# Performance work log

Measured on AMD Instinct MI355X. Metric: run time of the kernel, lower is better.

The kernel has to match this reference:

```python
import jax, jax.numpy as jnp
import numpy as np

N_NODES = 100000
N_EDGES = 1600000
N_GRAPHS = 64
FEAT = 64
EMB = 64
HID = 64
VOCAB = 32


def setup_inputs() -> dict:
    key = jax.random.key(0)
    ks = jax.random.split(key, 20)
    w = lambda k, sh: (jax.random.normal(k, sh, jnp.float32) * 0.05)
    x = jax.random.normal(ks[0], (N_NODES, FEAT), jnp.float32)
    edge_index = jax.random.randint(ks[1], (2, N_EDGES), 0, N_NODES, dtype=jnp.int32).astype(jnp.int64)
    batch = jnp.sort(jax.random.randint(ks[2], (N_NODES,), 0, N_GRAPHS, dtype=jnp.int32)).astype(jnp.int64)
    return {
        'x': x, 'edge_index': edge_index, 'batch': batch,
        # RGCN layer 1 (single relation): relation weight, root weight, bias
        'W1': w(ks[3], (FEAT, EMB)), 'root1': w(ks[4], (FEAT, EMB)), 'b1': w(ks[5], (EMB,)),
        # RGCN layer 2
        'W2': w(ks[6], (EMB, HID)), 'root2': w(ks[7], (EMB, HID)), 'b2': w(ks[8], (HID,)),
        # init_h / init_c linear heads
        'Wh': w(ks[9], (HID, HID)), 'bh': w(ks[10], (HID,)),
        'Wc': w(ks[11], (HID, HID)), 'bc': w(ks[12], (HID,)),
        # output layer
        'Wo': w(ks[13], (HID, VOCAB)), 'bo': w(ks[14], (VOCAB,)),
    }


def _rgcn(x, edge_index, W, root, b):
    # PyG RGCNConv with num_relations=1, aggr='mean':
    # out[i] = mean_{j in N(i)} (x[j] @ W) + x[i] @ root + b
    src, dst = edge_index[0], edge_index[1]
    msg = x[src] @ W                                    # [E, out] gather + small GEMM
    agg = jax.ops.segment_sum(msg, dst, num_segments=x.shape[0])
    cnt = jax.ops.segment_sum(jnp.ones((edge_index.shape[1],), x.dtype), dst, num_segments=x.shape[0])
    agg = agg / jnp.maximum(cnt, 1.0)[:, None]
    return agg + x @ root + b


def reference(x, edge_index, batch, W1, root1, b1, W2, root2, b2, Wh, bh, Wc, bc, Wo, bo):
    h = jax.nn.relu(_rgcn(x, edge_index, W1, root1, b1))
    h = jax.nn.relu(_rgcn(h, edge_index, W2, root2, b2))
    # global_mean_pool over graph-assignment vector `batch`
    summ = jax.ops.segment_sum(h, batch, num_segments=N_GRAPHS)
    cnt = jax.ops.segment_sum(jnp.ones((h.shape[0],), h.dtype), batch, num_segments=N_GRAPHS)
    pooled = summ / jnp.maximum(cnt, 1.0)[:, None]      # [G, HID]
    hidden = pooled @ Wh + bh
    cell = pooled @ Wc + bc
    logits = jax.nn.log_softmax(hidden @ Wo + bo, axis=1)
    return (logits, hidden, cell)
```

## Files before the change

kernel.cpp:

```cpp
#include <hip/hip_runtime.h>
#include <hip/hip_bf16.h>


typedef __attribute__((ext_vector_type(8))) short short8;
typedef __attribute__((ext_vector_type(4))) float f32x4;
typedef __attribute__((ext_vector_type(2))) float f32x2;

#define RB 9
#define MAXBINS 256
#define CAP 12288
#define BCAP 14336
#define CHUNK 8192

__device__ inline float bf2f(unsigned short h) {
    return __uint_as_float(((unsigned int)h) << 16);
}
__device__ inline float bflo(unsigned int u) { return __uint_as_float(u << 16); }
__device__ inline float bfhi(unsigned int u) { return __uint_as_float(u & 0xffff0000u); }
__device__ inline unsigned short f2bf(float f) {
    unsigned int u = __float_as_uint(f);
    u = (u + 0x7fffu + ((u >> 16) & 1u)) >> 16;
    return (unsigned short)u;
}

__device__ inline void build_bfrag(const float* __restrict__ W,
                                   const float* __restrict__ R,
                                   int q, int mm, short8 bfrag[8][2]) {
#pragma unroll
    for (int t = 0; t < 8; ++t) {
        const int n = t * 16 + mm;
        const float* P = (n < 64) ? (W + n) : (R + n - 64);
#pragma unroll
        for (int c = 0; c < 2; ++c) {
#pragma unroll
            for (int j = 0; j < 8; ++j) {
                const int k = c * 32 + q * 8 + j;
                bfrag[t][c][j] = (short)f2bf(P[k * 64]);
            }
        }
    }
}

__device__ inline void store_xw_fp8(unsigned char* __restrict__ xw8, int rowbase, int q,
                                    int t, int mm, const f32x4& accT, int N) {
#pragma unroll
    for (int r = 0; r < 4; ++r) {
        const float v0 = accT[r];
        const float v1 = __shfl_down(v0, 1);
        const float v2 = __shfl_down(v0, 2);
        const float v3 = __shfl_down(v0, 3);
        const int orow = rowbase + q * 4 + r;
        if (!(mm & 3) && orow < N) {
            unsigned int u = (unsigned int)__builtin_amdgcn_cvt_pk_fp8_f32(v0, v1, 0, false);
            u = (unsigned int)__builtin_amdgcn_cvt_pk_fp8_f32(v2, v3, (int)u, true);
            *(unsigned int*)&xw8[(size_t)orow * 64 + t * 16 + mm] = u;
        }
    }
}

__global__ __launch_bounds__(256) void bin_gemm1(const int* __restrict__ src,
                                                 const int* __restrict__ dst,
                                                 unsigned int* __restrict__ coarse,
                                                 int* __restrict__ gcur,
                                                 int E, int BINS, int nbBin,
                                                 const float* __restrict__ x,
                                                 const float* __restrict__ W1,
                                                 const float* __restrict__ R1,
                                                 const float* __restrict__ bias,
                                                 unsigned char* __restrict__ xw8,
                                                 unsigned short* __restrict__ xrb,
                                                 int N) {
    __shared__ int cnt[MAXBINS];
    __shared__ int incl[MAXBINS];
    __shared__ int bstart[MAXBINS];
    __shared__ int bcur[MAXBINS];
    __shared__ int gbase[MAXBINS];
    __shared__ unsigned int stage[CHUNK];
    __shared__ unsigned char binOf[CHUNK];

    const int tid = threadIdx.x;
    if (blockIdx.x >= (unsigned)nbBin) {
        const int gb = blockIdx.x - nbBin;
        if (gb == 0 && tid < 16)
            *(unsigned int*)&xw8[(size_t)N * 64 + tid * 4] = 0u;

        const int lane = tid & 63;
        const int q = lane >> 4;
        const int mm = lane & 15;

        short8 bfrag[8][2];
        build_bfrag(W1, R1, q, mm, bfrag);
        float bv[4];
#pragma unroll
        for (int tt = 0; tt < 4; ++tt) bv[tt] = bias[tt * 16 + mm];

        const int wid = tid >> 6;
        const int gw = gb * 4 + wid;
        const int nw = 1024 * 4;
        const int ntiles = N >> 4;

        for (int tile = gw; tile < ntiles; tile += nw) {
            const int row0 = tile << 4;
            const float* ap = &x[(size_t)(row0 + mm) * 64 + q * 8];
            const float4 f0 = *(const float4*)ap;
            const float4 f1 = *(const float4*)(ap + 4);
            const float4 f2 = *(const float4*)(ap + 32);
            const float4 f3 = *(const float4*)(ap + 36);
            short8 a0, a1;
            a0[0] = (short)f2bf(f0.x); a0[1] = (short)f2bf(f0.y);
            a0[2] = (short)f2bf(f0.z); a0[3] = (short)f2bf(f0.w);
            a0[4] = (short)f2bf(f1.x); a0[5] = (short)f2bf(f1.y);
            a0[6] = (short)f2bf(f1.z); a0[7] = (short)f2bf(f1.w);
            a1[0] = (short)f2bf(f2.x); a1[1] = (short)f2bf(f2.y);
            a1[2] = (short)f2bf(f2.z); a1[3] = (short)f2bf(f2.w);
            a1[4] = (short)f2bf(f3.x); a1[5] = (short)f2bf(f3.y);
            a1[6] = (short)f2bf(f3.z); a1[7] = (short)f2bf(f3.w);
            f32x4 acc[8];
#pragma unroll
            for (int t = 0; t < 8; ++t) {
                acc[t] = (f32x4){0.f, 0.f, 0.f, 0.f};
                acc[t] = __builtin_amdgcn_mfma_f32_16x16x32_bf16(a0, bfrag[t][0], acc[t], 0, 0, 0);
                acc[t] = __builtin_amdgcn_mfma_f32_16x16x32_bf16(a1, bfrag[t][1], acc[t], 0, 0, 0);
            }
#pragma unroll
            for (int t = 0; t < 4; ++t) store_xw_fp8(xw8, row0, q, t, mm, acc[t], N);
#pragma unroll
            for (int t = 4; t < 8; ++t) {
#pragma unroll
                for (int r = 0; r < 4; ++r) {
                    const float v = acc[t][r] + bv[t - 4];
                    const float vn = __shfl_down(v, 1);
                    if (!(mm & 1)) {
                        const unsigned int u = (unsigned int)f2bf(v) | ((unsigned int)f2bf(vn) << 16);
                        *(unsigned int*)&xrb[(size_t)(row0 + q * 4 + r) * 64 + (t - 4) * 16 + mm] = u;
                    }
                }
            }
        }
        return;
    }

    const int chunk0 = blockIdx.x * CHUNK;
    int myS[32], myD[32];
#pragma unroll
    for (int k = 0; k < 32; ++k) {
        const int idx = chunk0 + k * 256 + tid;
        if (idx < E) { myS[k] = src[idx]; myD[k] = dst[idx]; }
        else myD[k] = -1;
    }
    cnt[tid] = 0;
    __syncthreads();
#pragma unroll
    for (int k = 0; k < 32; ++k)
        if (myD[k] >= 0) atomicAdd(&cnt[myD[k] >> RB], 1);
    __syncthreads();
    incl[tid] = cnt[tid];
    __syncthreads();
    for (int off = 1; off < 256; off <<= 1) {
        int t = (tid >= off) ? incl[tid - off] : 0;
        __syncthreads();
        incl[tid] += t;
        __syncthreads();
    }
    bstart[tid] = incl[tid] - cnt[tid];
    bcur[tid] = incl[tid] - cnt[tid];
    __syncthreads();
#pragma unroll
    for (int k = 0; k < 32; ++k) {
        if (myD[k] >= 0) {
            const int b = myD[k] >> RB;
            const int pos = atomicAdd(&bcur[b], 1);
            stage[pos] = (unsigned int)myS[k] | ((unsigned int)(myD[k] & ((1 << RB) - 1)) << 17);
            binOf[pos] = (unsigned char)b;
        }
    }
    __syncthreads();
    if (tid < BINS && cnt[tid] > 0)
        gbase[tid] = tid * CAP + atomicAdd(&gcur[tid], cnt[tid]);
    __syncthreads();
    int total = E - chunk0;
    if (total > CHUNK) total = CHUNK;
    for (int idx = tid; idx < total; idx += 256) {
        const int b = binOf[idx];
        coarse[gbase[b] + (idx - bstart[b])] = stage[idx];
    }
}

__global__ __launch_bounds__(256) void finalize_csr(const unsigned int* __restrict__ coarse,
                                                    const int* __restrict__ gcur,
                                                    int* __restrict__ bucket,
                                                    int* __restrict__ pstart,
                                                    int* __restrict__ degarr,
                                                    int N, int BINS) {
    __shared__ int ncnt[512];
    __shared__ int pexcl[512];
    __shared__ int ncur[512];
    __shared__ int s2[256];

    const int tid = threadIdx.x;
    const int b = blockIdx.x;
    const int cb = gcur[b];
    const int base = b * BCAP;
    const unsigned int* reg = coarse + (size_t)b * CAP;
    const int node0 = b << RB;
    int nloc = N - node0;
    if (nloc > 512) nloc = 512;

    ncnt[tid] = 0; ncnt[tid + 256] = 0;
    __syncthreads();
    for (int idx = tid; idx < cb; idx += 256)
        atomicAdd(&ncnt[reg[idx] >> 17], 1);
    __syncthreads();
    const int p0 = (ncnt[2 * tid] + 15) & ~15;
    const int p1 = (ncnt[2 * tid + 1] + 15) & ~15;
    s2[tid] = p0 + p1;
    __syncthreads();
    for (int off = 1; off < 256; off <<= 1) {
        int t = (tid >= off) ? s2[tid - off] : 0;
        __syncthreads();
        s2[tid] += t;
        __syncthreads();
    }
    const int pairExcl = s2[tid] - (p0 + p1);
    pexcl[2 * tid] = pairExcl;
    pexcl[2 * tid + 1] = pairExcl + p0;
    ncur[2 * tid] = pairExcl;
    ncur[2 * tid + 1] = pairExcl + p0;
    __syncthreads();
    for (int i = tid; i < nloc; i += 256) {
        pstart[node0 + i] = base + pexcl[i];
        degarr[node0 + i] = ncnt[i];
        const int dg = ncnt[i];
        const int pd = (dg + 15) & ~15;
        for (int j = dg; j < pd; ++j) bucket[base + pexcl[i] + j] = N;
    }
    for (int idx = tid; idx < cb; idx += 256) {
        const unsigned int e = reg[idx];
        const int p = atomicAdd(&ncur[e >> 17], 1);
        bucket[base + p] = (int)(e & 0x1FFFFu);
    }
}

__global__ __launch_bounds__(256) void aggregate(const unsigned char* __restrict__ xw8,
                                                 const unsigned short* __restrict__ xrb,
                                                 const int* __restrict__ pstart,
                                                 const int* __restrict__ degarr,
                                                 const int* __restrict__ bucket,
                                                 unsigned short* __restrict__ outb,
                                                 int N) {
    const int lane = threadIdx.x & 63;
    const int quarter = lane >> 4;
    const int fl = lane & 15;
    const int wid = threadIdx.x >> 6;
    const int gw = blockIdx.x * 4 + wid;
    const int nw = gridDim.x * 4;

    for (int i = gw; i < N; i += nw) {
        const int r0 = pstart[i];
        const int dg = degarr[i];
        const int pdeg = (dg + 15) & ~15;
        float a0 = 0.f, a1 = 0.f, a2 = 0.f, a3 = 0.f;
        for (int base = 0; base < pdeg; base += 64) {
            const int rem = pdeg - base;
            const int s = (lane < rem) ? bucket[r0 + base + lane] : N;
            const int mm = rem < 64 ? rem : 64;
            for (int t = 0; t < mm; t += 16) {
                unsigned int u[4];
#pragma unroll
                for (int p = 0; p < 4; ++p) {
                    const int rr = __shfl(s, t + 4 * p + quarter);
                    u[p] = *(const unsigned int*)&xw8[(size_t)rr * 64 + fl * 4];
                }
#pragma unroll
                for (int p = 0; p < 4; ++p) {
                    const f32x2 lo = __builtin_amdgcn_cvt_pk_f32_fp8(u[p], false);
                    const f32x2 hi = __builtin_amdgcn_cvt_pk_f32_fp8(u[p], true);
                    a0 += lo.x; a1 += lo.y; a2 += hi.x; a3 += hi.y;
                }
            }
        }
        a0 += __shfl_xor(a0, 16); a1 += __shfl_xor(a1, 16);
        a2 += __shfl_xor(a2, 16); a3 += __shfl_xor(a3, 16);
        a0 += __shfl_xor(a0, 32); a1 += __shfl_xor(a1, 32);
        a2 += __shfl_xor(a2, 32); a3 += __shfl_xor(a3, 32);

        const float inv = 1.0f / (float)(dg > 0 ? dg : 1);
        if (quarter == 0) {
            const uint2 ur = *(const uint2*)&xrb[(size_t)i * 64 + fl * 4];
            const float o0 = fmaxf(a0 * inv + bflo(ur.x), 0.f);
            const float o1 = fmaxf(a1 * inv + bfhi(ur.x), 0.f);
            const float o2 = fmaxf(a2 * inv + bflo(ur.y), 0.f);
            const float o3 = fmaxf(a3 * inv + bfhi(ur.y), 0.f);
            uint2 w;
            w.x = (unsigned int)f2bf(o0) | ((unsigned int)f2bf(o1) << 16);
            w.y = (unsigned int)f2bf(o2) | ((unsigned int)f2bf(o3) << 16);
            *(uint2*)&outb[(size_t)i * 64 + fl * 4] = w;
        }
    }
}

__global__ __launch_bounds__(256) void gemm_xwr2(const unsigned short* __restrict__ xin,
                                                 const float* __restrict__ W2,
                                                 const float* __restrict__ R2,
                                                 const float* __restrict__ bias,
                                                 unsigned char* __restrict__ xw8,
                                                 unsigned short* __restrict__ xrb,
                                                 int M) {
    if (blockIdx.x == 0 && threadIdx.x < 16)
        *(unsigned int*)&xw8[(size_t)M * 64 + threadIdx.x * 4] = 0u;

    const int lane = threadIdx.x & 63;
    const int q = lane >> 4;
    const int mm = lane & 15;

    short8 bfrag[8][2];
    build_bfrag(W2, R2, q, mm, bfrag);
    float bv[4];
#pragma unroll
    for (int tt = 0; tt < 4; ++tt) bv[tt] = bias[tt * 16 + mm];

    const int wid = threadIdx.x >> 6;
    const int gw = blockIdx.x * 4 + wid;
    const int nw = gridDim.x * 4;
    const int ntiles = M >> 4;

    for (int tile = gw; tile < ntiles; tile += nw) {
        const int row0 = tile << 4;
        const short8 a0 = *(const short8*)&xin[(size_t)(row0 + mm) * 64 + q * 8];
        const short8 a1 = *(const short8*)&xin[(size_t)(row0 + mm) * 64 + 32 + q * 8];
        f32x4 acc[8];
#pragma unroll
        for (int t = 0; t < 8; ++t) {
            acc[t] = (f32x4){0.f, 0.f, 0.f, 0.f};
            acc[t] = __builtin_amdgcn_mfma_f32_16x16x32_bf16(a0, bfrag[t][0], acc[t], 0, 0, 0);
            acc[t] = __builtin_amdgcn_mfma_f32_16x16x32_bf16(a1, bfrag[t][1], acc[t], 0, 0, 0);
        }
#pragma unroll
        for (int t = 0; t < 4; ++t) store_xw_fp8(xw8, row0, q, t, mm, acc[t], M);
#pragma unroll
        for (int t = 4; t < 8; ++t) {
#pragma unroll
            for (int r = 0; r < 4; ++r) {
                const float v = acc[t][r] + bv[t - 4];
                const float vn = __shfl_down(v, 1);
                if (!(mm & 1)) {
                    const unsigned int u = (unsigned int)f2bf(v) | ((unsigned int)f2bf(vn) << 16);
                    *(unsigned int*)&xrb[(size_t)(row0 + q * 4 + r) * 64 + (t - 4) * 16 + mm] = u;
                }
            }
        }
    }
}

__global__ __launch_bounds__(256) void pool_kernel(const unsigned short* __restrict__ h,
                                                   const int* __restrict__ batch,
                                                   float* __restrict__ pooled, int N) {
    __shared__ float red[16][64];
    __shared__ int bnds[2];
    const int gph = blockIdx.x;
    if (threadIdx.x < 2) {
        const int target = gph + threadIdx.x;
        int lo = 0, hi = N;
        while (lo < hi) {
            int mid = (lo + hi) >> 1;
            if (batch[mid] < target) lo = mid + 1; else hi = mid;
        }
        bnds[threadIdx.x] = lo;
    }
    __syncthreads();
    const int r0 = bnds[0], r1 = bnds[1];
    const int f = threadIdx.x & 15;
    const int r = threadIdx.x >> 4;
    float4 acc = {0.f, 0.f, 0.f, 0.f};
    for (int row = r0 + r; row < r1; row += 16) {
        const ushort4 v = *(const ushort4*)&h[(size_t)row * 64 + f * 4];
        acc.x += bf2f(v.x); acc.y += bf2f(v.y);
        acc.z += bf2f(v.z); acc.w += bf2f(v.w);
    }
    red[r][f * 4 + 0] = acc.x; red[r][f * 4 + 1] = acc.y;
    red[r][f * 4 + 2] = acc.z; red[r][f * 4 + 3] = acc.w;
    __syncthreads();
    if (threadIdx.x < 64) {
        float s = 0.f;
        for (int j = 0; j < 16; ++j) s += red[j][threadIdx.x];
        const int cnt = r1 - r0;
        const float invc = 1.0f / (float)(cnt > 0 ? cnt : 1);
        pooled[gph * 64 + threadIdx.x] = s * invc;
    }
}

__global__ __launch_bounds__(256) void head_kernel(const float* __restrict__ pooled,
                                                   const float* __restrict__ Wh,
                                                   const float* __restrict__ bh,
                                                   const float* __restrict__ Wc,
                                                   const float* __restrict__ bc,
                                                   const float* __restrict__ Wo,
                                                   const float* __restrict__ bo,
                                                   float* __restrict__ out) {
    __shared__ float pm[4096];
    __shared__ float Ws[4096];
    __shared__ float Cs[4096];
    __shared__ float hid[4096];
    const int t = threadIdx.x;

    for (int idx = t; idx < 1024; idx += 256) {
        ((float4*)pm)[idx] = ((const float4*)pooled)[idx];
        ((float4*)Ws)[idx] = ((const float4*)Wh)[idx];
        ((float4*)Cs)[idx] = ((const float4*)Wc)[idx];
    }
    __syncthreads();

    const int w = t >> 6;
    const int l = t & 63;
    const float bhv = bh[l], bcv = bc[l];
    float ah[16], ac[16];
#pragma unroll
    for (int i = 0; i < 16; ++i) { ah[i] = bhv; ac[i] = bcv; }
    const float* pmw = pm + ((w << 4) << 6);
#pragma unroll 4
    for (int k = 0; k < 64; ++k) {
        const float wv = Ws[(k << 6) + l];
        const float cv = Cs[(k << 6) + l];
#pragma unroll
        for (int i = 0; i < 16; ++i) {
            const float p = pmw[(i << 6) + k];
            ah[i] = fmaf(p, wv, ah[i]);
            ac[i] = fmaf(p, cv, ac[i]);
        }
    }
#pragma unroll
    for (int i = 0; i < 16; ++i) {
        const int g = (w << 4) + i;
        hid[(g << 6) + l] = ah[i];
        out[2048 + (g << 6) + l] = ah[i];
        out[6144 + (g << 6) + l] = ac[i];
    }
    __syncthreads();
    for (int idx = t; idx < 512; idx += 256)
        ((float4*)Ws)[idx] = ((const float4*)Wo)[idx];
    __syncthreads();

    const int v = l & 31;
    const int gh = l >> 5;
    const int g0 = ((w << 1) + gh) << 3;
    const float bov = bo[v];
    float lgacc[8];
#pragma unroll
    for (int i = 0; i < 8; ++i) lgacc[i] = bov;
#pragma unroll 4
    for (int k = 0; k < 64; ++k) {
        const float wv = Ws[(k << 5) + v];
#pragma unroll
        for (int i = 0; i < 8; ++i)
            lgacc[i] = fmaf(hid[((g0 + i) << 6) + k], wv, lgacc[i]);
    }
    float* lg = pm;
#pragma unroll
    for (int i = 0; i < 8; ++i) lg[((g0 + i) << 5) + v] = lgacc[i];
    __syncthreads();

    const int g = t >> 2;
    const int vs = (t & 3) << 3;
    const float* row = lg + (g << 5);
    float mx = -3.4e38f;
#pragma unroll
    for (int j = 0; j < 8; ++j) mx = fmaxf(mx, row[vs + j]);
    mx = fmaxf(mx, __shfl_xor(mx, 1));
    mx = fmaxf(mx, __shfl_xor(mx, 2));
    float s = 0.f;
#pragma unroll
    for (int j = 0; j < 8; ++j) s += __expf(row[vs + j] - mx);
    s += __shfl_xor(s, 1);
    s += __shfl_xor(s, 2);
    const float lse = mx + __logf(s);
#pragma unroll
    for (int j = 0; j < 8; ++j) out[(g << 5) + vs + j] = row[vs + j] - lse;
}

extern "C" void kernel_launch(void* const* d_in, const int* in_sizes, int n_in,
                              void* d_out, int out_size, void* d_ws, size_t ws_size,
                              hipStream_t stream) {
    const float* x = (const float*)d_in[0];
    const int* ei = (const int*)d_in[1];
    const int* batch = (const int*)d_in[2];
    const float* W1 = (const float*)d_in[3];
    const float* root1 = (const float*)d_in[4];
    const float* b1 = (const float*)d_in[5];
    const float* W2 = (const float*)d_in[6];
    const float* root2 = (const float*)d_in[7];
    const float* b2 = (const float*)d_in[8];
    const float* Wh = (const float*)d_in[9];
    const float* bh = (const float*)d_in[10];
    const float* Wc = (const float*)d_in[11];
    const float* bc = (const float*)d_in[12];
    const float* Wo = (const float*)d_in[13];
    const float* bo = (const float*)d_in[14];
    float* out = (float*)d_out;

    const int N = in_sizes[0] / 64;
    const int E = in_sizes[1] / 2;
    const int* srcp = ei;
    const int* dstp = ei + E;
    const int BINS = (N + (1 << RB) - 1) >> RB;

    char* ws = (char*)d_ws;
    size_t off = 0;
    auto alloc = [&](size_t bytes) -> void* {
        void* p = ws + off;
        off += (bytes + 255) & ~(size_t)255;
        return p;
    };
    int* pstart = (int*)alloc((size_t)N * 4);
    int* degarr = (int*)alloc((size_t)N * 4);
    int* bucket = (int*)alloc(((size_t)BINS * BCAP + 256) * 4);
    unsigned int* coarse = (unsigned int*)alloc((size_t)BINS * CAP * 4);
    unsigned short* h1 = (unsigned short*)alloc((size_t)N * 64 * 2);
    unsigned short* h2 = (unsigned short*)alloc((size_t)N * 64 * 2);
    unsigned char* xw8 = (unsigned char*)alloc((size_t)(N + 1) * 64);
    unsigned char* xw8b = (unsigned char*)alloc((size_t)(N + 1) * 64);
    unsigned short* xrb = (unsigned short*)alloc((size_t)N * 64 * 2);
    unsigned short* xrb2 = (unsigned short*)alloc((size_t)N * 64 * 2);
    float* pooled = (float*)alloc(4096 * 4);
    int* gcur = (int*)alloc(MAXBINS * 4);

    const int nbBin = (E + CHUNK - 1) / CHUNK;

    hipMemsetAsync(gcur, 0, MAXBINS * 4, stream);
    bin_gemm1<<<nbBin + 1024, 256, 0, stream>>>(srcp, dstp, coarse, gcur, E, BINS, nbBin,
                                                x, W1, root1, b1, xw8, xrb, N);
    finalize_csr<<<BINS, 256, 0, stream>>>(coarse, gcur, bucket, pstart, degarr, N, BINS);
    aggregate<<<4096, 256, 0, stream>>>(xw8, xrb, pstart, degarr, bucket, h1, N);
    gemm_xwr2<<<1024, 256, 0, stream>>>(h1, W2, root2, b2, xw8b, xrb2, N);
    aggregate<<<4096, 256, 0, stream>>>(xw8b, xrb2, pstart, degarr, bucket, h2, N);
    pool_kernel<<<64, 256, 0, stream>>>(h2, batch, pooled, N);
    head_kernel<<<1, 256, 0, stream>>>(pooled, Wh, bh, Wc, bc, Wo, bo, out);
}
```

Baseline: 272.0 us.

## Fuse layer-1 aggregation with layer-2 GEMM and layer-2 aggregation with pooling

Layer-1 neighbour aggregation now writes each 16-row tile into LDS and immediately feeds it to the MFMA transform for layer 2, removing the h1 buffer round trip. Layer-2 aggregation accumulates per-graph sums over contiguous node ranges and flushes them with atomics, removing h2 and the separate pooling kernel; the head kernel now computes graph counts and normalizes. This cuts global traffic and launches but serializes 16 rows per wave in the first fused kernel, which may reduce latency hiding, and introduces float atomics.

Result: slower. 348.5 us (+28.1%).

```diff
diff --git a/kernel.cpp b/kernel.cpp
--- a/kernel.cpp
+++ b/kernel.cpp
@@ -241,21 +241,149 @@
     }
 }
 
-__global__ __launch_bounds__(256) void aggregate(const unsigned char* __restrict__ xw8,
+__global__ __launch_bounds__(256) void agg1_gemm2(const unsigned char* __restrict__ xw8,
+                                                  const unsigned short* __restrict__ xrb,
+                                                  const int* __restrict__ pstart,
+                                                  const int* __restrict__ degarr,
+                                                  const int* __restrict__ bucket,
+                                                  const float* __restrict__ W2,
+                                                  const float* __restrict__ R2,
+                                                  const float* __restrict__ bias,
+                                                  unsigned char* __restrict__ xw8b,
+                                                  unsigned short* __restrict__ xrb2,
+                                                  int N) {
+    if (blockIdx.x == 0 && threadIdx.x < 16)
+        *(unsigned int*)&xw8b[(size_t)N * 64 + threadIdx.x * 4] = 0u;
+
+    __shared__ unsigned short tile[4][16 * 72];
+
+    const int lane = threadIdx.x & 63;
+    const int quarter = lane >> 4;
+    const int fl = lane & 15;
+    const int wid = threadIdx.x >> 6;
+
+    short8 bfrag[8][2];
+    build_bfrag(W2, R2, quarter, fl, bfrag);
+    float bv[4];
+#pragma unroll
+    for (int tt = 0; tt < 4; ++tt) bv[tt] = bias[tt * 16 + fl];
+
+    const int gw = blockIdx.x * 4 + wid;
+    const int nw = gridDim.x * 4;
+    const int ntiles = (N + 15) >> 4;
+    unsigned short* my = tile[wid];
+
+    for (int tl = gw; tl < ntiles; tl += nw) {
+        const int row0 = tl << 4;
+        for (int r = 0; r < 16; ++r) {
+            const int i = row0 + r;
+            float a0 = 0.f, a1 = 0.f, a2 = 0.f, a3 = 0.f;
+            int dg = 0;
+            if (i < N) {
+                const int r0 = pstart[i];
+                dg = degarr[i];
+                const int pdeg = (dg + 15) & ~15;
+                for (int base = 0; base < pdeg; base += 64) {
+                    const int rem = pdeg - base;
+                    const int s = (lane < rem) ? bucket[r0 + base + lane] : N;
+                    const int mx = rem < 64 ? rem : 64;
+                    for (int tq = 0; tq < mx; tq += 16) {
+                        unsigned int u[4];
+#pragma unroll
+                        for (int p = 0; p < 4; ++p) {
+                            const int rr = __shfl(s, tq + 4 * p + quarter);
+                            u[p] = *(const unsigned int*)&xw8[(size_t)rr * 64 + fl * 4];
+                        }
+#pragma unroll
+                        for (int p = 0; p < 4; ++p) {
+                            const f32x2 lo = __builtin_amdgcn_cvt_pk_f32_fp8(u[p], false);
+                            const f32x2 hi = __builtin_amdgcn_cvt_pk_f32_fp8(u[p], true);
+                            a0 += lo.x; a1 += lo.y; a2 += hi.x; a3 += hi.y;
+                        }
+                    }
+                }
+                a0 += __shfl_xor(a0, 16); a1 += __shfl_xor(a1, 16);
+                a2 += __shfl_xor(a2, 16); a3 += __shfl_xor(a3, 16);
+                a0 += __shfl_xor(a0, 32); a1 += __shfl_xor(a1, 32);
+                a2 += __shfl_xor(a2, 32); a3 += __shfl_xor(a3, 32);
+            }
+            if (quarter == 0) {
+                uint2 w = {0u, 0u};
+                if (i < N) {
+                    const float inv = 1.0f / (float)(dg > 0 ? dg : 1);
+                    const uint2 ur = *(const uint2*)&xrb[(size_t)i * 64 + fl * 4];
+                    const float o0 = fmaxf(a0 * inv + bflo(ur.x), 0.f);
+                    const float o1 = fmaxf(a1 * inv + bfhi(ur.x), 0.f);
+                    const float o2 = fmaxf(a2 * inv + bflo(ur.y), 0.f);
+                    const float o3 = fmaxf(a3 * inv + bfhi(ur.y), 0.f);
+                    w.x = (unsigned int)f2bf(o0) | ((unsigned int)f2bf(o1) << 16);
+                    w.y = (unsigned int)f2bf(o2) | ((unsigned int)f2bf(o3) << 16);
+                }
+                *(uint2*)&my[r * 72 + fl * 4] = w;
+            }
+        }
+        asm volatile("s_waitcnt lgkmcnt(0)" ::: "memory");
+        __builtin_amdgcn_sched_barrier(0);
+        const short8 a0v = *(const short8*)&my[fl * 72 + quarter * 8];
+        const short8 a1v = *(const short8*)&my[fl * 72 + 32 + quarter * 8];
+        f32x4 acc[8];
+#pragma unroll
+        for (int t = 0; t < 8; ++t) {
+            acc[t] = (f32x4){0.f, 0.f, 0.f, 0.f};
+            acc[t] = __builtin_amdgcn_mfma_f32_16x16x32_bf16(a0v, bfrag[t][0], acc[t], 0, 0, 0);
+            acc[t] = __builtin_amdgcn_mfma_f32_16x16x32_bf16(a1v, bfrag[t][1], acc[t], 0, 0, 0);
+        }
+#pragma unroll
+        for (int t = 0; t < 4; ++t) store_xw_fp8(xw8b, row0, quarter, t, fl, acc[t], N);
+#pragma unroll
+        for (int t = 4; t < 8; ++t) {
+#pragma unroll
+            for (int r2 = 0; r2 < 4; ++r2) {
+                const float v = acc[t][r2] + bv[t - 4];
+                const float vn = __shfl_down(v, 1);
+                const int orow = row0 + quarter * 4 + r2;
+                if (!(fl & 1) && orow < N) {
+                    const unsigned int u = (unsigned int)f2bf(v) | ((unsigned int)f2bf(vn) << 16);
+                    *(unsigned int*)&xrb2[(size_t)orow * 64 + (t - 4) * 16 + fl] = u;
+                }
+            }
+        }
+    }
+}
+
+__global__ __launch_bounds__(256) void agg2_pool(const unsigned char* __restrict__ xw8,
                                                  const unsigned short* __restrict__ xrb,
                                                  const int* __restrict__ pstart,
                                                  const int* __restrict__ degarr,
                                                  const int* __restrict__ bucket,
-                                                 unsigned short* __restrict__ outb,
+                                                 const int* __restrict__ batch,
+                                                 float* __restrict__ gsum,
                                                  int N) {
     const int lane = threadIdx.x & 63;
     const int quarter = lane >> 4;
     const int fl = lane & 15;
     const int wid = threadIdx.x >> 6;
     const int gw = blockIdx.x * 4 + wid;
-    const int nw = gridDim.x * 4;
-
-    for (int i = gw; i < N; i += nw) {
+    const int tw = gridDim.x * 4;
+    const int C = (N + tw - 1) / tw;
+    const int i0 = gw * C;
+    int i1 = i0 + C;
+    if (i1 > N) i1 = N;
+
+    float s0 = 0.f, s1 = 0.f, s2 = 0.f, s3 = 0.f;
+    int curg = -1;
+    for (int i = i0; i < i1; ++i) {
+        const int g = batch[i];
+        if (g != curg) {
+            if (curg >= 0 && quarter == 0) {
+                atomicAdd(&gsum[curg * 64 + fl * 4 + 0], s0);
+                atomicAdd(&gsum[curg * 64 + fl * 4 + 1], s1);
+                atomicAdd(&gsum[curg * 64 + fl * 4 + 2], s2);
+                atomicAdd(&gsum[curg * 64 + fl * 4 + 3], s3);
+            }
+            s0 = s1 = s2 = s3 = 0.f;
+            curg = g;
+        }
         const int r0 = pstart[i];
         const int dg = degarr[i];
         const int pdeg = (dg + 15) & ~15;
@@ -263,12 +391,12 @@
         for (int base = 0; base < pdeg; base += 64) {
             const int rem = pdeg - base;
             const int s = (lane < rem) ? bucket[r0 + base + lane] : N;
-            const int mm = rem < 64 ? rem : 64;
-            for (int t = 0; t < mm; t += 16) {
+            const int mx = rem < 64 ? rem : 64;
+            for (int tq = 0; tq < mx; tq += 16) {
                 unsigned int u[4];
 #pragma unroll
                 for (int p = 0; p < 4; ++p) {
-                    const int rr = __shfl(s, t + 4 * p + quarter);
+                    const int rr = __shfl(s, tq + 4 * p + quarter);
                     u[p] = *(const unsigned int*)&xw8[(size_t)rr * 64 + fl * 4];
                 }
 #pragma unroll
@@ -284,127 +412,55 @@
         a0 += __shfl_xor(a0, 32); a1 += __shfl_xor(a1, 32);
         a2 += __shfl_xor(a2, 32); a3 += __shfl_xor(a3, 32);
 
-        const float inv = 1.0f / (float)(dg > 0 ? dg : 1);
         if (quarter == 0) {
+            const float inv = 1.0f / (float)(dg > 0 ? dg : 1);
             const uint2 ur = *(const uint2*)&xrb[(size_t)i * 64 + fl * 4];
-            const float o0 = fmaxf(a0 * inv + bflo(ur.x), 0.f);
-            const float o1 = fmaxf(a1 * inv + bfhi(ur.x), 0.f);
-            const float o2 = fmaxf(a2 * inv + bflo(ur.y), 0.f);
-            const float o3 = fmaxf(a3 * inv + bfhi(ur.y), 0.f);
-            uint2 w;
-            w.x = (unsigned int)f2bf(o0) | ((unsigned int)f2bf(o1) << 16);
-            w.y = (unsigned int)f2bf(o2) | ((unsigned int)f2bf(o3) << 16);
-            *(uint2*)&outb[(size_t)i * 64 + fl * 4] = w;
-        }
-    }
-}
-
-__global__ __launch_bounds__(256) void gemm_xwr2(const unsigned short* __restrict__ xin,
-                                                 const float* __restrict__ W2,
-                                                 const float* __restrict__ R2,
-                                                 const float* __restrict__ bias,
-                                                 unsigned char* __restrict__ xw8,
-                                                 unsigned short* __restrict__ xrb,
-                                                 int M) {
-    if (blockIdx.x == 0 && threadIdx.x < 16)
-        *(unsigned int*)&xw8[(size_t)M * 64 + threadIdx.x * 4] = 0u;
-
-    const int lane = threadIdx.x & 63;
-    const int q = lane >> 4;
-    const int mm = lane & 15;
-
-    short8 bfrag[8][2];
-    build_bfrag(W2, R2, q, mm, bfrag);
-    float bv[4];
-#pragma unroll
-    for (int tt = 0; tt < 4; ++tt) bv[tt] = bias[tt * 16 + mm];
-
-    const int wid = threadIdx.x >> 6;
-    const int gw = blockIdx.x * 4 + wid;
-    const int nw = gridDim.x * 4;
-    const int ntiles = M >> 4;
-
-    for (int tile = gw; tile < ntiles; tile += nw) {
-        const int row0 = tile << 4;
-        const short8 a0 = *(const short8*)&xin[(size_t)(row0 + mm) * 64 + q * 8];
-        const short8 a1 = *(const short8*)&xin[(size_t)(row0 + mm) * 64 + 32 + q * 8];
-        f32x4 acc[8];
-#pragma unroll
-        for (int t = 0; t < 8; ++t) {
-            acc[t] = (f32x4){0.f, 0.f, 0.f, 0.f};
-            acc[t] = __builtin_amdgcn_mfma_f32_16x16x32_bf16(a0, bfrag[t][0], acc[t], 0, 0, 0);
-            acc[t] = __builtin_amdgcn_mfma_f32_16x16x32_bf16(a1, bfrag[t][1], acc[t], 0, 0, 0);
-        }
-#pragma unroll
-        for (int t = 0; t < 4; ++t) store_xw_fp8(xw8, row0, q, t, mm, acc[t], M);
-#pragma unroll
-        for (int t = 4; t < 8; ++t) {
-#pragma unroll
-            for (int r = 0; r < 4; ++r) {
-                const float v = acc[t][r] + bv[t - 4];
-                const float vn = __shfl_down(v, 1);
-                if (!(mm & 1)) {
-                    const unsigned int u = (unsigned int)f2bf(v) | ((unsigned int)f2bf(vn) << 16);
-                    *(unsigned int*)&xrb[(size_t)(row0 + q * 4 + r) * 64 + (t - 4) * 16 + mm] = u;
-                }
-            }
-        }
-    }
-}
-
-__global__ __launch_bounds__(256) void pool_kernel(const unsigned short* __restrict__ h,
+            s0 += fmaxf(a0 * inv + bflo(ur.x), 0.f);
+            s1 += fmaxf(a1 * inv + bfhi(ur.x), 0.f);
+            s2 += fmaxf(a2 * inv + bflo(ur.y), 0.f);
+            s3 += fmaxf(a3 * inv + bfhi(ur.y), 0.f);
+        }
+    }
+    if (curg >= 0 && quarter == 0) {
+        atomicAdd(&gsum[curg * 64 + fl * 4 + 0], s0);
+        atomicAdd(&gsum[curg * 64 + fl * 4 + 1], s1);
+        atomicAdd(&gsum[curg * 64 + fl * 4 + 2], s2);
+        atomicAdd(&gsum[curg * 64 + fl * 4 + 3], s3);
+    }
+}
+
+__global__ __launch_bounds__(256) void head_kernel(const float* __restrict__ gsum,
                                                    const int* __restrict__ batch,
-                                                   float* __restrict__ pooled, int N) {
-    __shared__ float red[16][64];
-    __shared__ int bnds[2];
-    const int gph = blockIdx.x;
-    if (threadIdx.x < 2) {
-        const int target = gph + threadIdx.x;
-        int lo = 0, hi = N;
-        while (lo < hi) {
-            int mid = (lo + hi) >> 1;
-            if (batch[mid] < target) lo = mid + 1; else hi = mid;
-        }
-        bnds[threadIdx.x] = lo;
-    }
-    __syncthreads();
-    const int r0 = bnds[0], r1 = bnds[1];
-    const int f = threadIdx.x & 15;
-    const int r = threadIdx.x >> 4;
-    float4 acc = {0.f, 0.f, 0.f, 0.f};
-    for (int row = r0 + r; row < r1; row += 16) {
-        const ushort4 v = *(const ushort4*)&h[(size_t)row * 64 + f * 4];
-        acc.x += bf2f(v.x); acc.y += bf2f(v.y);
-        acc.z += bf2f(v.z); acc.w += bf2f(v.w);
-    }
-    red[r][f * 4 + 0] = acc.x; red[r][f * 4 + 1] = acc.y;
-    red[r][f * 4 + 2] = acc.z; red[r][f * 4 + 3] = acc.w;
-    __syncthreads();
-    if (threadIdx.x < 64) {
-        float s = 0.f;
-        for (int j = 0; j < 16; ++j) s += red[j][threadIdx.x];
-        const int cnt = r1 - r0;
-        const float invc = 1.0f / (float)(cnt > 0 ? cnt : 1);
-        pooled[gph * 64 + threadIdx.x] = s * invc;
-    }
-}
-
-__global__ __launch_bounds__(256) void head_kernel(const float* __restrict__ pooled,
                                                    const float* __restrict__ Wh,
                                                    const float* __restrict__ bh,
                                                    const float* __restrict__ Wc,
                                                    const float* __restrict__ bc,
                                                    const float* __restrict__ Wo,
                                                    const float* __restrict__ bo,
-                                                   float* __restrict__ out) {
+                                                   float* __restrict__ out, int N) {
     __shared__ float pm[4096];
     __shared__ float Ws[4096];
     __shared__ float Cs[4096];
     __shared__ float hid[4096];
+    __shared__ int bnds[65];
     const int t = threadIdx.x;
 
+    if (t < 65) {
+        int lo = 0, hi = N;
+        while (lo < hi) {
+            int mid = (lo + hi) >> 1;
+            if (batch[mid] < t) lo = mid + 1; else hi = mid;
+        }
+        bnds[t] = lo;
+    }
+    __syncthreads();
     for (int idx = t; idx < 1024; idx += 256) {
-        ((float4*)pm)[idx] = ((const float4*)pooled)[idx];
+        const int g = idx >> 4;
+        const int c = bnds[g + 1] - bnds[g];
+        const float inv = 1.0f / (float)(c > 0 ? c : 1);
+        float4 v = ((const float4*)gsum)[idx];
+        v.x *= inv; v.y *= inv; v.z *= inv; v.w *= inv;
+        ((float4*)pm)[idx] = v;
         ((float4*)Ws)[idx] = ((const float4*)Wh)[idx];
         ((float4*)Cs)[idx] = ((const float4*)Wc)[idx];
     }
@@ -514,24 +570,22 @@
     int* degarr = (int*)alloc((size_t)N * 4);
     int* bucket = (int*)alloc(((size_t)BINS * BCAP + 256) * 4);
     unsigned int* coarse = (unsigned int*)alloc((size_t)BINS * CAP * 4);
-    unsigned short* h1 = (unsigned short*)alloc((size_t)N * 64 * 2);
-    unsigned short* h2 = (unsigned short*)alloc((size_t)N * 64 * 2);
     unsigned char* xw8 = (unsigned char*)alloc((size_t)(N + 1) * 64);
     unsigned char* xw8b = (unsigned char*)alloc((size_t)(N + 1) * 64);
     unsigned short* xrb = (unsigned short*)alloc((size_t)N * 64 * 2);
     unsigned short* xrb2 = (unsigned short*)alloc((size_t)N * 64 * 2);
-    float* pooled = (float*)alloc(4096 * 4);
     int* gcur = (int*)alloc(MAXBINS * 4);
+    float* gsum = (float*)alloc(64 * 64 * 4);
 
     const int nbBin = (E + CHUNK - 1) / CHUNK;
-
-    hipMemsetAsync(gcur, 0, MAXBINS * 4, stream);
+    const int ntiles = (N + 15) >> 4;
+
+    hipMemsetAsync(gcur, 0, MAXBINS * 4 + 64 * 64 * 4, stream);
     bin_gemm1<<<nbBin + 1024, 256, 0, stream>>>(srcp, dstp, coarse, gcur, E, BINS, nbBin,
                                                 x, W1, root1, b1, xw8, xrb, N);
     finalize_csr<<<BINS, 256, 0, stream>>>(coarse, gcur, bucket, pstart, degarr, N, BINS);
-    aggregate<<<4096, 256, 0, stream>>>(xw8, xrb, pstart, degarr, bucket, h1, N);
-    gemm_xwr2<<<1024, 256, 0, stream>>>(h1, W2, root2, b2, xw8b, xrb2, N);
-    aggregate<<<4096, 256, 0, stream>>>(xw8b, xrb2, pstart, degarr, bucket, h2, N);
-    pool_kernel<<<64, 256, 0, stream>>>(h2, batch, pooled, N);
-    head_kernel<<<1, 256, 0, stream>>>(pooled, Wh, bh, Wc, bc, Wo, bo, out);
-}
+    agg1_gemm2<<<(ntiles + 3) / 4, 256, 0, stream>>>(xw8, xrb, pstart, degarr, bucket,
+                                                     W2, root2, b2, xw8b, xrb2, N);
+    agg2_pool<<<2048, 256, 0, stream>>>(xw8b, xrb2, pstart, degarr, bucket, batch, gsum, N);
+    head_kernel<<<1, 256, 0, stream>>>(gsum, batch, Wh, bh, Wc, bc, Wo, bo, out, N);
+}
```

## Batch four nodes per wavefront in aggregate and split pooling across blocks

Applied to the files above, without the earlier changes.

The aggregate kernel now processes four destination nodes per wavefront at once, issuing their neighbour gathers together to raise memory-level parallelism. Loop trip counts are padded to the largest degree in the group, adding some redundant loads of the zero row. Pooling is split into four blocks per graph that accumulate partial sums with float atomics. Division by node count moves into the head kernel, which recomputes graph boundaries.

After: 275.6 us. No clear change (+1.3%).

```diff
diff --git a/kernel.cpp b/kernel.cpp
--- a/kernel.cpp
+++ b/kernel.cpp
@@ -255,46 +255,80 @@
     const int gw = blockIdx.x * 4 + wid;
     const int nw = gridDim.x * 4;
 
-    for (int i = gw; i < N; i += nw) {
-        const int r0 = pstart[i];
-        const int dg = degarr[i];
-        const int pdeg = (dg + 15) & ~15;
-        float a0 = 0.f, a1 = 0.f, a2 = 0.f, a3 = 0.f;
-        for (int base = 0; base < pdeg; base += 64) {
-            const int rem = pdeg - base;
-            const int s = (lane < rem) ? bucket[r0 + base + lane] : N;
-            const int mm = rem < 64 ? rem : 64;
-            for (int t = 0; t < mm; t += 16) {
-                unsigned int u[4];
-#pragma unroll
-                for (int p = 0; p < 4; ++p) {
-                    const int rr = __shfl(s, t + 4 * p + quarter);
-                    u[p] = *(const unsigned int*)&xw8[(size_t)rr * 64 + fl * 4];
+    for (int i = gw; i < N; i += 4 * nw) {
+        int idxs[4], r0[4], dg[4], pd[4];
+#pragma unroll
+        for (int j = 0; j < 4; ++j) {
+            idxs[j] = i + j * nw;
+            const bool hasJ = idxs[j] < N;
+            const int ii = hasJ ? idxs[j] : i;
+            r0[j] = pstart[ii];
+            dg[j] = hasJ ? degarr[ii] : 0;
+            pd[j] = (dg[j] + 15) & ~15;
+        }
+        int pdM = pd[0];
+#pragma unroll
+        for (int j = 1; j < 4; ++j) pdM = pd[j] > pdM ? pd[j] : pdM;
+
+        float acc[4][4];
+#pragma unroll
+        for (int j = 0; j < 4; ++j)
+#pragma unroll
+            for (int c = 0; c < 4; ++c) acc[j][c] = 0.f;
+
+        for (int base = 0; base < pdM; base += 64) {
+            int s[4];
+#pragma unroll
+            for (int j = 0; j < 4; ++j) {
+                const int rem = pd[j] - base;
+                s[j] = (lane < rem) ? bucket[r0[j] + base + lane] : N;
+            }
+            int mx = pdM - base;
+            if (mx > 64) mx = 64;
+            for (int t = 0; t < mx; t += 16) {
+                unsigned int u[4][4];
+#pragma unroll
+                for (int j = 0; j < 4; ++j)
+#pragma unroll
+                    for (int p = 0; p < 4; ++p) {
+                        const int rr = __shfl(s[j], t + 4 * p + quarter);
+                        u[j][p] = *(const unsigned int*)&xw8[(size_t)rr * 64 + fl * 4];
+                    }
+#pragma unroll
+                for (int j = 0; j < 4; ++j)
+#pragma unroll
+                    for (int p = 0; p < 4; ++p) {
+                        const f32x2 lo = __builtin_amdgcn_cvt_pk_f32_fp8(u[j][p], false);
+                        const f32x2 hi = __builtin_amdgcn_cvt_pk_f32_fp8(u[j][p], true);
+                        acc[j][0] += lo.x; acc[j][1] += lo.y;
+                        acc[j][2] += hi.x; acc[j][3] += hi.y;
+                    }
+            }
+        }
+#pragma unroll
+        for (int j = 0; j < 4; ++j)
+#pragma unroll
+            for (int c = 0; c < 4; ++c) {
+                acc[j][c] += __shfl_xor(acc[j][c], 16);
+                acc[j][c] += __shfl_xor(acc[j][c], 32);
+            }
+
+        if (quarter == 0) {
+#pragma unroll
+            for (int j = 0; j < 4; ++j) {
+                if (idxs[j] < N) {
+                    const float inv = 1.0f / (float)(dg[j] > 0 ? dg[j] : 1);
+                    const uint2 ur = *(const uint2*)&xrb[(size_t)idxs[j] * 64 + fl * 4];
+                    const float o0 = fmaxf(acc[j][0] * inv + bflo(ur.x), 0.f);
+                    const float o1 = fmaxf(acc[j][1] * inv + bfhi(ur.x), 0.f);
+                    const float o2 = fmaxf(acc[j][2] * inv + bflo(ur.y), 0.f);
+                    const float o3 = fmaxf(acc[j][3] * inv + bfhi(ur.y), 0.f);
+                    uint2 w;
+                    w.x = (unsigned int)f2bf(o0) | ((unsigned int)f2bf(o1) << 16);
+                    w.y = (unsigned int)f2bf(o2) | ((unsigned int)f2bf(o3) << 16);
+                    *(uint2*)&outb[(size_t)idxs[j] * 64 + fl * 4] = w;
                 }
-#pragma unroll
-                for (int p = 0; p < 4; ++p) {
-                    const f32x2 lo = __builtin_amdgcn_cvt_pk_f32_fp8(u[p], false);
-                    const f32x2 hi = __builtin_amdgcn_cvt_pk_f32_fp8(u[p], true);
-                    a0 += lo.x; a1 += lo.y; a2 += hi.x; a3 += hi.y;
-                }
-            }
-        }
-        a0 += __shfl_xor(a0, 16); a1 += __shfl_xor(a1, 16);
-        a2 += __shfl_xor(a2, 16); a3 += __shfl_xor(a3, 16);
-        a0 += __shfl_xor(a0, 32); a1 += __shfl_xor(a1, 32);
-        a2 += __shfl_xor(a2, 32); a3 += __shfl_xor(a3, 32);
-
-        const float inv = 1.0f / (float)(dg > 0 ? dg : 1);
-        if (quarter == 0) {
-            const uint2 ur = *(const uint2*)&xrb[(size_t)i * 64 + fl * 4];
-            const float o0 = fmaxf(a0 * inv + bflo(ur.x), 0.f);
-            const float o1 = fmaxf(a1 * inv + bfhi(ur.x), 0.f);
-            const float o2 = fmaxf(a2 * inv + bflo(ur.y), 0.f);
-            const float o3 = fmaxf(a3 * inv + bfhi(ur.y), 0.f);
-            uint2 w;
-            w.x = (unsigned int)f2bf(o0) | ((unsigned int)f2bf(o1) << 16);
-            w.y = (unsigned int)f2bf(o2) | ((unsigned int)f2bf(o3) << 16);
-            *(uint2*)&outb[(size_t)i * 64 + fl * 4] = w;
+            }
         }
     }
 }
@@ -354,10 +388,11 @@
 
 __global__ __launch_bounds__(256) void pool_kernel(const unsigned short* __restrict__ h,
                                                    const int* __restrict__ batch,
-                                                   float* __restrict__ pooled, int N) {
+                                                   float* __restrict__ gsum, int N) {
     __shared__ float red[16][64];
     __shared__ int bnds[2];
-    const int gph = blockIdx.x;
+    const int gph = blockIdx.x >> 2;
+    const int part = blockIdx.x & 3;
     if (threadIdx.x < 2) {
         const int target = gph + threadIdx.x;
         int lo = 0, hi = N;
@@ -368,11 +403,13 @@
         bnds[threadIdx.x] = lo;
     }
     __syncthreads();
-    const int r0 = bnds[0], r1 = bnds[1];
+    const int r0 = bnds[0], tot = bnds[1] - bnds[0];
+    const int pr0 = r0 + (tot * part) / 4;
+    const int pr1 = r0 + (tot * (part + 1)) / 4;
     const int f = threadIdx.x & 15;
     const int r = threadIdx.x >> 4;
     float4 acc = {0.f, 0.f, 0.f, 0.f};
-    for (int row = r0 + r; row < r1; row += 16) {
+    for (int row = pr0 + r; row < pr1; row += 16) {
         const ushort4 v = *(const ushort4*)&h[(size_t)row * 64 + f * 4];
         acc.x += bf2f(v.x); acc.y += bf2f(v.y);
         acc.z += bf2f(v.z); acc.w += bf2f(v.w);
@@ -383,28 +420,42 @@
     if (threadIdx.x < 64) {
         float s = 0.f;
         for (int j = 0; j < 16; ++j) s += red[j][threadIdx.x];
-        const int cnt = r1 - r0;
-        const float invc = 1.0f / (float)(cnt > 0 ? cnt : 1);
-        pooled[gph * 64 + threadIdx.x] = s * invc;
-    }
-}
-
-__global__ __launch_bounds__(256) void head_kernel(const float* __restrict__ pooled,
+        atomicAdd(&gsum[gph * 64 + threadIdx.x], s);
+    }
+}
+
+__global__ __launch_bounds__(256) void head_kernel(const float* __restrict__ gsum,
+                                                   const int* __restrict__ batch,
                                                    const float* __restrict__ Wh,
                                                    const float* __restrict__ bh,
                                                    const float* __restrict__ Wc,
                                                    const float* __restrict__ bc,
                                                    const float* __restrict__ Wo,
                                                    const float* __restrict__ bo,
-                                                   float* __restrict__ out) {
+                                                   float* __restrict__ out, int N) {
     __shared__ float pm[4096];
     __shared__ float Ws[4096];
     __shared__ float Cs[4096];
     __shared__ float hid[4096];
+    __shared__ int bnds[65];
     const int t = threadIdx.x;
 
+    if (t < 65) {
+        int lo = 0, hi = N;
+        while (lo < hi) {
+            int mid = (lo + hi) >> 1;
+            if (batch[mid] < t) lo = mid + 1; else hi = mid;
+        }
+        bnds[t] = lo;
+    }
+    __syncthreads();
     for (int idx = t; idx < 1024; idx += 256) {
-        ((float4*)pm)[idx] = ((const float4*)pooled)[idx];
+        const int g = idx >> 4;
+        const int c = bnds[g + 1] - bnds[g];
+        const float inv = 1.0f / (float)(c > 0 ? c : 1);
+        float4 v = ((const float4*)gsum)[idx];
+        v.x *= inv; v.y *= inv; v.z *= inv; v.w *= inv;
+        ((float4*)pm)[idx] = v;
         ((float4*)Ws)[idx] = ((const float4*)Wh)[idx];
         ((float4*)Cs)[idx] = ((const float4*)Wc)[idx];
     }
@@ -520,18 +571,18 @@
     unsigned char* xw8b = (unsigned char*)alloc((size_t)(N + 1) * 64);
     unsigned short* xrb = (unsigned short*)alloc((size_t)N * 64 * 2);
     unsigned short* xrb2 = (unsigned short*)alloc((size_t)N * 64 * 2);
-    float* pooled = (float*)alloc(4096 * 4);
     int* gcur = (int*)alloc(MAXBINS * 4);
+    float* gsum = (float*)alloc(4096 * 4);
 
     const int nbBin = (E + CHUNK - 1) / CHUNK;
 
-    hipMemsetAsync(gcur, 0, MAXBINS * 4, stream);
+    hipMemsetAsync(gcur, 0, MAXBINS * 4 + 4096 * 4, stream);
     bin_gemm1<<<nbBin + 1024, 256, 0, stream>>>(srcp, dstp, coarse, gcur, E, BINS, nbBin,
                                                 x, W1, root1, b1, xw8, xrb, N);
     finalize_csr<<<BINS, 256, 0, stream>>>(coarse, gcur, bucket, pstart, degarr, N, BINS);
     aggregate<<<4096, 256, 0, stream>>>(xw8, xrb, pstart, degarr, bucket, h1, N);
     gemm_xwr2<<<1024, 256, 0, stream>>>(h1, W2, root2, b2, xw8b, xrb2, N);
     aggregate<<<4096, 256, 0, stream>>>(xw8b, xrb2, pstart, degarr, bucket, h2, N);
-    pool_kernel<<<64, 256, 0, stream>>>(h2, batch, pooled, N);
-    head_kernel<<<1, 256, 0, stream>>>(pooled, Wh, bh, Wc, bc, Wo, bo, out);
-}
+    pool_kernel<<<256, 256, 0, stream>>>(h2, batch, gsum, N);
+    head_kernel<<<1, 256, 0, stream>>>(gsum, batch, Wh, bh, Wc, bc, Wo, bo, out, N);
+}
```
